# Performance work log

Hardware: AMD Instinct MI355X
Metric: run time of the kernel (lower is better)

## Reference

```python
import jax, jax.numpy as jnp
import numpy as np

N_NODES = 100000


def sage_conv(x, src, dst, W_l, b_l, W_r, n_nodes):
    # mean-aggregate source neighbors onto destination nodes (PyG SAGEConv, aggr='mean')
    agg = jax.ops.segment_sum(x[src], dst, num_segments=n_nodes)          # [N, d_in]
    cnt = jax.ops.segment_sum(jnp.ones((src.shape[0], 1), x.dtype), dst,
                              num_segments=n_nodes)                        # [N, 1]
    agg = agg / jnp.maximum(cnt, 1.0)  # isolated nodes -> 0, as in scatter-mean
    # out = lin_l(agg) + lin_r(x); bias lives in lin_l
    return agg @ W_l + b_l + x @ W_r


def setup_inputs() -> dict:
    key = jax.random.key(0)
    ks = jax.random.split(key, 12)
    d_in, h1, h2, h3 = 256, 256, 128, 1
    x = jax.random.normal(ks[0], (N_NODES, d_in), dtype=jnp.float32)
    edge_index = jax.random.randint(ks[1], (2, 1600000), 0, N_NODES, dtype=jnp.int64)

    def lin(k, din, dout):
        s = 1.0 / np.sqrt(din)
        return jax.random.uniform(k, (din, dout), jnp.float32, -s, s)

    return {
        "x": x,
        "edge_index": edge_index,
        "Wl1": lin(ks[2], d_in, h1), "bl1": jnp.zeros((h1,), jnp.float32), "Wr1": lin(ks[3], d_in, h1),
        "Wl2": lin(ks[4], h1, h2),  "bl2": jnp.zeros((h2,), jnp.float32), "Wr2": lin(ks[5], h1, h2),
        "Wl3": lin(ks[6], h2, h3),  "bl3": jnp.zeros((h3,), jnp.float32), "Wr3": lin(ks[7], h2, h3),
    }


def reference(x, edge_index, Wl1, bl1, Wr1, Wl2, bl2, Wr2, Wl3, bl3, Wr3):
    src, dst = edge_index[0], edge_index[1]
    n = x.shape[0]
    h = jax.nn.relu(sage_conv(x, src, dst, Wl1, bl1, Wr1, n))
    h = jax.nn.relu(sage_conv(h, src, dst, Wl2, bl2, Wr2, n))
    out = sage_conv(h, src, dst, Wl3, bl3, Wr3, n)
    return out  # [N, 1]
```

## Files before the change

### kernel.cpp

```cpp
#include <hip/hip_runtime.h>
#include <hip/hip_bf16.h>


typedef __attribute__((ext_vector_type(8))) short short8;
typedef __attribute__((ext_vector_type(4))) float f32x4;

__device__ __forceinline__ unsigned short f2b(float f) {
    __hip_bfloat16 h = __float2bfloat16(f);
    return *reinterpret_cast<unsigned short*>(&h);
}
__device__ __forceinline__ float b2f(unsigned short u) {
    union { unsigned int i; float f; } v; v.i = ((unsigned int)u) << 16; return v.f;
}

__global__ __launch_bounds__(256) void prep_fused(
    const float* __restrict__ x, unsigned short* __restrict__ xb,
    const float* __restrict__ Wl1, const float* __restrict__ Wr1,
    const float* __restrict__ Wl2, const float* __restrict__ Wr2,
    unsigned short* __restrict__ Wl1s, unsigned short* __restrict__ Wr1s,
    unsigned short* __restrict__ Wl2s, unsigned short* __restrict__ Wr2s,
    const int* __restrict__ dst, int* __restrict__ deg,
    unsigned short* __restrict__ rank, int E)
{
    const int b = blockIdx.x;
    const int tid = threadIdx.x;
    if (b < 25000) {
        const int i = b * 256 + tid;
        float4 v = *(const float4*)(x + (size_t)i * 4);
        ushort4 o;
        o.x = f2b(v.x); o.y = f2b(v.y); o.z = f2b(v.z); o.w = f2b(v.w);
        *(ushort4*)(xb + (size_t)i * 4) = o;
        if (tid < 64) {
            const int e = b * 64 + tid;
            if (e < E) rank[e] = (unsigned short)atomicAdd(&deg[dst[e]], 1);
        }
    } else {
        const float* W; unsigned short* O; int base, hs;
        if (b < 25256)      { W = Wl1; O = Wl1s; base = b - 25000; hs = 8; }
        else if (b < 25512) { W = Wr1; O = Wr1s; base = b - 25256; hs = 8; }
        else if (b < 25640) { W = Wl2; O = Wl2s; base = b - 25512; hs = 7; }
        else                { W = Wr2; O = Wr2s; base = b - 25640; hs = 7; }
        const int i = base * 256 + tid;
        const int k = i >> hs;
        const int h = i & ((1 << hs) - 1);
        O[((size_t)(((k >> 3) << hs) + h) << 3) + (k & 7)] = f2b(W[i]);
    }
}

__global__ __launch_bounds__(256) void scan_phaseA(int* __restrict__ a,
                                                   int* __restrict__ blockSums, int n) {
    __shared__ int sh[256];
    const int tid = threadIdx.x;
    const int base = blockIdx.x * 1024 + tid * 4;
    int v[4];
    #pragma unroll
    for (int i = 0; i < 4; ++i) v[i] = (base + i < n) ? a[base + i] : 0;
    int tsum = v[0] + v[1] + v[2] + v[3];
    sh[tid] = tsum;
    __syncthreads();
    for (int off = 1; off < 256; off <<= 1) {
        int t = (tid >= off) ? sh[tid - off] : 0;
        __syncthreads();
        sh[tid] += t;
        __syncthreads();
    }
    int run = sh[tid] - tsum;
    #pragma unroll
    for (int i = 0; i < 4; ++i) {
        if (base + i < n) a[base + i] = run;
        run += v[i];
    }
    if (tid == 255) blockSums[blockIdx.x] = sh[255];
}

__global__ __launch_bounds__(256) void scan_phaseB(int* __restrict__ bs, int nb) {
    __shared__ int sh[256];
    const int tid = threadIdx.x;
    int v = (tid < nb) ? bs[tid] : 0;
    sh[tid] = v;
    __syncthreads();
    for (int off = 1; off < 256; off <<= 1) {
        int t = (tid >= off) ? sh[tid - off] : 0;
        __syncthreads();
        sh[tid] += t;
        __syncthreads();
    }
    if (tid < nb) bs[tid] = sh[tid] - v;
}

__global__ __launch_bounds__(256) void scan_phaseC(int* __restrict__ a,
                                                   const int* __restrict__ bs, int n) {
    const int base = blockIdx.x * 1024 + threadIdx.x * 4;
    const int add = bs[blockIdx.x];
    #pragma unroll
    for (int i = 0; i < 4; ++i)
        if (base + i < n) a[base + i] += add;
}

__global__ __launch_bounds__(256) void gemm_l1_fill(
    const unsigned short* __restrict__ Xb,
    const unsigned short* __restrict__ Wsw_l,
    const unsigned short* __restrict__ Wsw_r,
    const float* __restrict__ bias,
    unsigned short* __restrict__ Tout,
    unsigned short* __restrict__ Abase,
    int M,
    const int* __restrict__ src, const int* __restrict__ dst,
    const int* __restrict__ starts, const unsigned short* __restrict__ rank,
    int* __restrict__ csr, int E)
{
    const int grp = blockIdx.x / 3;
    const int rem = blockIdx.x - grp * 3;
    const int tid = threadIdx.x;

    if (rem != 0) {
        const int e = (grp * 2 + rem - 1) * 256 + tid;
        if (e < E) csr[starts[dst[e]] + (int)rank[e]] = src[e];
        return;
    }

    const int H = 256;
    const int wid = tid >> 6;
    const int lane = tid & 63;
    const int quad = lane >> 4;
    const int l15 = lane & 15;
    const int col0 = (grp & 3) << 6;
    const int m0 = (grp >> 2) * 128 + wid * 32;

    const unsigned short* aptr[2];
    #pragma unroll
    for (int mt = 0; mt < 2; ++mt) {
        int r = m0 + mt * 16 + l15;
        if (r > M - 1) r = M - 1;
        aptr[mt] = Xb + ((size_t)r << 8) + (quad << 3);
    }
    const unsigned short* bptr[8];
    #pragma unroll
    for (int nt = 0; nt < 4; ++nt) {
        const int col = col0 + nt * 16 + l15;
        bptr[nt]     = Wsw_l + (((size_t)quad * H + col) << 3);
        bptr[nt + 4] = Wsw_r + (((size_t)quad * H + col) << 3);
    }

    const f32x4 zero = {0.f, 0.f, 0.f, 0.f};
    f32x4 acc[2][8];
    #pragma unroll
    for (int mt = 0; mt < 2; ++mt)
        #pragma unroll
        for (int nt = 0; nt < 8; ++nt) acc[mt][nt] = zero;

    #pragma unroll 2
    for (int ks = 0; ks < 8; ++ks) {
        short8 af[2], bf[8];
        #pragma unroll
        for (int mt = 0; mt < 2; ++mt)
            af[mt] = *(const short8*)(aptr[mt] + ks * 32);
        #pragma unroll
        for (int nt = 0; nt < 8; ++nt)
            bf[nt] = *(const short8*)(bptr[nt] + (size_t)ks * 32 * H);
        #pragma unroll
        for (int mt = 0; mt < 2; ++mt)
            #pragma unroll
            for (int nt = 0; nt < 8; ++nt)
                acc[mt][nt] = __builtin_amdgcn_mfma_f32_16x16x32_bf16(
                    af[mt], bf[nt], acc[mt][nt], 0, 0, 0);
    }

    #pragma unroll
    for (int nt = 0; nt < 4; ++nt) {
        const int colg = col0 + nt * 16 + l15;
        const float bb = bias[colg];
        #pragma unroll
        for (int mt = 0; mt < 2; ++mt) {
            const int gmb = m0 + mt * 16 + quad * 4;
            #pragma unroll
            for (int r = 0; r < 4; ++r) {
                if (gmb + r < M) {
                    Tout [(size_t)(gmb + r) * H + colg] = f2b(acc[mt][nt][r]);
                    Abase[(size_t)(gmb + r) * H + colg] = f2b(acc[mt][nt + 4][r] + bb);
                }
            }
        }
    }
}

__global__ __launch_bounds__(256) void agg256_b(
    const int* __restrict__ endoff, const int* __restrict__ csr,
    const unsigned short* __restrict__ T,
    const unsigned short* __restrict__ Abase, unsigned short* __restrict__ Xout,
    int N, int E)
{
    const int node = (int)((blockIdx.x * 256 + threadIdx.x) >> 5);
    const int lane = threadIdx.x & 31;
    if (node >= N) return;
    const int beg = endoff[node];
    const int end = (node + 1 < N) ? endoff[node + 1] : E;
    float s[8] = {0.f, 0.f, 0.f, 0.f, 0.f, 0.f, 0.f, 0.f};
    int p = beg;
    for (; p + 8 <= end; p += 8) {
        int idx[8];
        #pragma unroll
        for (int u = 0; u < 8; ++u) idx[u] = csr[p + u];
        short8 v[8];
        #pragma unroll
        for (int u = 0; u < 8; ++u)
            v[u] = *(const short8*)(T + ((size_t)idx[u] << 8) + (lane << 3));
        #pragma unroll
        for (int j = 0; j < 8; ++j) {
            float t0 = b2f((unsigned short)v[0][j]) + b2f((unsigned short)v[1][j]);
            float t1 = b2f((unsigned short)v[2][j]) + b2f((unsigned short)v[3][j]);
            float t2 = b2f((unsigned short)v[4][j]) + b2f((unsigned short)v[5][j]);
            float t3 = b2f((unsigned short)v[6][j]) + b2f((unsigned short)v[7][j]);
            s[j] += (t0 + t1) + (t2 + t3);
        }
    }
    if (p + 4 <= end) {
        const int a = csr[p], b = csr[p + 1], c = csr[p + 2], d = csr[p + 3];
        const short8 v0 = *(const short8*)(T + ((size_t)a << 8) + (lane << 3));
        const short8 v1 = *(const short8*)(T + ((size_t)b << 8) + (lane << 3));
        const short8 v2 = *(const short8*)(T + ((size_t)c << 8) + (lane << 3));
        const short8 v3 = *(const short8*)(T + ((size_t)d << 8) + (lane << 3));
        #pragma unroll
        for (int j = 0; j < 8; ++j)
            s[j] += (b2f((unsigned short)v0[j]) + b2f((unsigned short)v1[j]))
                  + (b2f((unsigned short)v2[j]) + b2f((unsigned short)v3[j]));
        p += 4;
    }
    for (; p < end; ++p) {
        const short8 v = *(const short8*)(T + ((size_t)csr[p] << 8) + (lane << 3));
        #pragma unroll
        for (int j = 0; j < 8; ++j) s[j] += b2f((unsigned short)v[j]);
    }
    const float w = 1.0f / fmaxf((float)(end - beg), 1.0f);
    const short8 bu = *(const short8*)(Abase + ((size_t)node << 8) + (lane << 3));
    short8 o;
    #pragma unroll
    for (int j = 0; j < 8; ++j)
        o[j] = (short)f2b(fmaxf(b2f((unsigned short)bu[j]) + s[j] * w, 0.f));
    *(short8*)(Xout + ((size_t)node << 8) + (lane << 3)) = o;
}

__global__ __launch_bounds__(256) void gemm_bf16(
    const unsigned short* __restrict__ Xb,
    const unsigned short* __restrict__ Wsw_l,
    const unsigned short* __restrict__ Wsw_r,
    const float* __restrict__ bias,
    unsigned short* __restrict__ Tout,
    unsigned short* __restrict__ Abase,
    int M, int H)
{
    const int tid = threadIdx.x;
    const int wid = tid >> 6;
    const int lane = tid & 63;
    const int quad = lane >> 4;
    const int l15 = lane & 15;

    const int col0 = blockIdx.x << 6;
    const int m0 = blockIdx.y * 128 + wid * 32;

    const unsigned short* aptr[2];
    #pragma unroll
    for (int mt = 0; mt < 2; ++mt) {
        int r = m0 + mt * 16 + l15;
        if (r > M - 1) r = M - 1;
        aptr[mt] = Xb + ((size_t)r << 8) + (quad << 3);
    }
    const unsigned short* bptr[8];
    #pragma unroll
    for (int nt = 0; nt < 4; ++nt) {
        const int col = col0 + nt * 16 + l15;
        bptr[nt]     = Wsw_l + (((size_t)quad * H + col) << 3);
        bptr[nt + 4] = Wsw_r + (((size_t)quad * H + col) << 3);
    }

    const f32x4 zero = {0.f, 0.f, 0.f, 0.f};
    f32x4 acc[2][8];
    #pragma unroll
    for (int mt = 0; mt < 2; ++mt)
        #pragma unroll
        for (int nt = 0; nt < 8; ++nt) acc[mt][nt] = zero;

    #pragma unroll 2
    for (int ks = 0; ks < 8; ++ks) {
        short8 af[2], bf[8];
        #pragma unroll
        for (int mt = 0; mt < 2; ++mt)
            af[mt] = *(const short8*)(aptr[mt] + ks * 32);
        #pragma unroll
        for (int nt = 0; nt < 8; ++nt)
            bf[nt] = *(const short8*)(bptr[nt] + (size_t)ks * 32 * H);
        #pragma unroll
        for (int mt = 0; mt < 2; ++mt)
            #pragma unroll
            for (int nt = 0; nt < 8; ++nt)
                acc[mt][nt] = __builtin_amdgcn_mfma_f32_16x16x32_bf16(
                    af[mt], bf[nt], acc[mt][nt], 0, 0, 0);
    }

    #pragma unroll
    for (int nt = 0; nt < 4; ++nt) {
        const int colg = col0 + nt * 16 + l15;
        const float bb = bias[colg];
        #pragma unroll
        for (int mt = 0; mt < 2; ++mt) {
            const int gmb = m0 + mt * 16 + quad * 4;
            #pragma unroll
            for (int r = 0; r < 4; ++r) {
                if (gmb + r < M) {
                    Tout [(size_t)(gmb + r) * H + colg] = f2b(acc[mt][nt][r]);
                    Abase[(size_t)(gmb + r) * H + colg] = f2b(acc[mt][nt + 4][r] + bb);
                }
            }
        }
    }
}

__global__ __launch_bounds__(256) void agg_gemv3(
    const int* __restrict__ endoff, const int* __restrict__ csr,
    const unsigned short* __restrict__ T, const unsigned short* __restrict__ Ab,
    const float* __restrict__ Wl, const float* __restrict__ Wr,
    const float* __restrict__ b,
    float* __restrict__ t3, float* __restrict__ out, int N, int E)
{
    const int node = (int)((blockIdx.x * 256 + threadIdx.x) >> 5);
    const int lane = threadIdx.x & 31;
    if (node >= N) return;
    const int beg = endoff[node];
    const int end = (node + 1 < N) ? endoff[node + 1] : E;
    float s0 = 0.f, s1 = 0.f, s2 = 0.f, s3 = 0.f;
    int p = beg;
    for (; p + 8 <= end; p += 8) {
        int idx[8];
        #pragma unroll
        for (int u = 0; u < 8; ++u) idx[u] = csr[p + u];
        ushort4 v[8];
        #pragma unroll
        for (int u = 0; u < 8; ++u)
            v[u] = *(const ushort4*)(T + ((size_t)idx[u] << 7) + (lane << 2));
        #pragma unroll
        for (int u = 0; u < 8; ++u) {
            s0 += b2f(v[u].x); s1 += b2f(v[u].y);
            s2 += b2f(v[u].z); s3 += b2f(v[u].w);
        }
    }
    if (p + 4 <= end) {
        const int a = csr[p], bb = csr[p + 1], c = csr[p + 2], d = csr[p + 3];
        ushort4 v0 = *(const ushort4*)(T + ((size_t)a << 7) + (lane << 2));
        ushort4 v1 = *(const ushort4*)(T + ((size_t)bb << 7) + (lane << 2));
        ushort4 v2 = *(const ushort4*)(T + ((size_t)c << 7) + (lane << 2));
        ushort4 v3 = *(const ushort4*)(T + ((size_t)d << 7) + (lane << 2));
        s0 += (b2f(v0.x) + b2f(v1.x)) + (b2f(v2.x) + b2f(v3.x));
        s1 += (b2f(v0.y) + b2f(v1.y)) + (b2f(v2.y) + b2f(v3.y));
        s2 += (b2f(v0.z) + b2f(v1.z)) + (b2f(v2.z) + b2f(v3.z));
        s3 += (b2f(v0.w) + b2f(v1.w)) + (b2f(v2.w) + b2f(v3.w));
        p += 4;
    }
    for (; p < end; ++p) {
        ushort4 v = *(const ushort4*)(T + ((size_t)csr[p] << 7) + (lane << 2));
        s0 += b2f(v.x); s1 += b2f(v.y); s2 += b2f(v.z); s3 += b2f(v.w);
    }
    const float w = 1.0f / fmaxf((float)(end - beg), 1.0f);
    const ushort4 bu = *(const ushort4*)(Ab + ((size_t)node << 7) + (lane << 2));
    const float h0 = fmaxf(b2f(bu.x) + s0 * w, 0.f);
    const float h1 = fmaxf(b2f(bu.y) + s1 * w, 0.f);
    const float h2 = fmaxf(b2f(bu.z) + s2 * w, 0.f);
    const float h3 = fmaxf(b2f(bu.w) + s3 * w, 0.f);

    const float4 wl = *(const float4*)(Wl + (lane << 2));
    const float4 wr = *(const float4*)(Wr + (lane << 2));
    float dl = h0 * wl.x + h1 * wl.y + h2 * wl.z + h3 * wl.w;
    float dr = h0 * wr.x + h1 * wr.y + h2 * wr.z + h3 * wr.w;
    #pragma unroll
    for (int off = 16; off > 0; off >>= 1) {
        dl += __shfl_down(dl, off, 64);
        dr += __shfl_down(dr, off, 64);
    }
    if (lane == 0) {
        t3[node] = dl;
        out[node] = dr + b[0];
    }
}

__global__ __launch_bounds__(256) void agg1(
    const int* __restrict__ endoff, const int* __restrict__ csr,
    const float* __restrict__ t3, float* __restrict__ out, int N, int E)
{
    const int i = blockIdx.x * blockDim.x + threadIdx.x;
    if (i >= N) return;
    const int beg = endoff[i];
    const int end = (i + 1 < N) ? endoff[i + 1] : E;
    int p = beg;
    float s = 0.f;
    for (; p + 4 <= end; p += 4)
        s += (t3[csr[p]] + t3[csr[p + 1]]) + (t3[csr[p + 2]] + t3[csr[p + 3]]);
    for (; p < end; ++p) s += t3[csr[p]];
    out[i] += s / fmaxf((float)(end - beg), 1.0f);
}

extern "C" void kernel_launch(void* const* d_in, const int* in_sizes, int n_in,
                              void* d_out, int out_size, void* d_ws, size_t ws_size,
                              hipStream_t stream) {
    const float* x   = (const float*)d_in[0];
    const int*   ei  = (const int*)d_in[1];
    const float* Wl1 = (const float*)d_in[2];
    const float* bl1 = (const float*)d_in[3];
    const float* Wr1 = (const float*)d_in[4];
    const float* Wl2 = (const float*)d_in[5];
    const float* bl2 = (const float*)d_in[6];
    const float* Wr2 = (const float*)d_in[7];
    const float* Wl3 = (const float*)d_in[8];
    const float* bl3 = (const float*)d_in[9];
    const float* Wr3 = (const float*)d_in[10];
    float* out = (float*)d_out;

    const int N = in_sizes[0] / 256;
    const int E = in_sizes[1] / 2;
    const int* src = ei;
    const int* dst = ei + E;

    char* W = (char*)d_ws;
    const size_t MB512 = (size_t)100000 * 512;
    unsigned short* X1b = (unsigned short*)(W);
    unsigned short* T1b = (unsigned short*)(W + MB512);
    unsigned short* A1b = (unsigned short*)(W + 2 * MB512);
    unsigned short* X2b = (unsigned short*)(W);
    unsigned short* T2b = (unsigned short*)(W + MB512);
    unsigned short* A2b = (unsigned short*)(W + MB512 + MB512 / 2);
    char* S = W + 3 * MB512;
    int*   endoff = (int*)(S);
    int*   bsums  = (int*)(S + (size_t)N * 4);
    float* t3     = (float*)(S + (size_t)N * 4 + 1024);
    int*   csr    = (int*)(S + (size_t)N * 8 + 1024);
    unsigned short* Wl1s = (unsigned short*)(S + (size_t)N * 8 + 1024 + (size_t)E * 4);
    unsigned short* Wr1s = Wl1s + 65536;
    unsigned short* Wl2s = Wr1s + 65536;
    unsigned short* Wr2s = Wl2s + 32768;
    unsigned short* rank = Wr2s + 32768;

    hipMemsetAsync(endoff, 0, (size_t)N * sizeof(int), stream);
    prep_fused<<<25768, 256, 0, stream>>>(
        x, X1b, Wl1, Wr1, Wl2, Wr2, Wl1s, Wr1s, Wl2s, Wr2s,
        dst, endoff, rank, E);
    const int nScanBlocks = (N + 1023) / 1024;
    scan_phaseA<<<nScanBlocks, 256, 0, stream>>>(endoff, bsums, N);
    scan_phaseB<<<1, 256, 0, stream>>>(bsums, nScanBlocks);
    scan_phaseC<<<nScanBlocks, 256, 0, stream>>>(endoff, bsums, N);

    gemm_l1_fill<<<3128 * 3, 256, 0, stream>>>(X1b, Wl1s, Wr1s, bl1, T1b, A1b, N,
                                               src, dst, endoff, rank, csr, E);

    agg256_b<<<(N * 32 + 255) / 256, 256, 0, stream>>>(endoff, csr, T1b, A1b, X2b, N, E);
    gemm_bf16<<<dim3(2, (N + 127) / 128), 256, 0, stream>>>(X2b, Wl2s, Wr2s, bl2,
                                                            T2b, A2b, N, 128);

    agg_gemv3<<<(N * 32 + 255) / 256, 256, 0, stream>>>(endoff, csr, T2b, A2b,
                                                        Wl3, Wr3, bl3, t3, out, N, E);
    agg1<<<(N + 255) / 256, 256, 0, stream>>>(endoff, csr, t3, out, N, E);
}
```

Before: 570.1 us.

## Stage layer-1 GEMM tiles in LDS via direct global-to-LDS loads, remap blocks

```diff
diff --git a/kernel.cpp b/kernel.cpp
--- a/kernel.cpp
+++ b/kernel.cpp
@@ -11,6 +11,13 @@
 }
 __device__ __forceinline__ float b2f(unsigned short u) {
     union { unsigned int i; float f; } v; v.i = ((unsigned int)u) << 16; return v.f;
+}
+
+__device__ __forceinline__ void gload_lds16(const unsigned short* g, unsigned short* l) {
+    __builtin_amdgcn_global_load_lds(
+        (const __attribute__((address_space(1))) unsigned int*)(const void*)g,
+        (__attribute__((address_space(3))) unsigned int*)(void*)l,
+        16, 0, 0);
 }
 
 __global__ __launch_bounds__(256) void prep_fused(
@@ -109,8 +116,9 @@
     const int* __restrict__ starts, const unsigned short* __restrict__ rank,
     int* __restrict__ csr, int E)
 {
-    const int grp = blockIdx.x / 3;
-    const int rem = blockIdx.x - grp * 3;
+    const int bid = (blockIdx.x & 7) * 1173 + (blockIdx.x >> 3);
+    const int grp = bid / 3;
+    const int rem = bid - grp * 3;
     const int tid = threadIdx.x;
 
     if (rem != 0) {
@@ -119,27 +127,34 @@
         return;
     }
 
-    const int H = 256;
+    __shared__ unsigned short smem[16384];
+
     const int wid = tid >> 6;
     const int lane = tid & 63;
     const int quad = lane >> 4;
     const int l15 = lane & 15;
     const int col0 = (grp & 3) << 6;
-    const int m0 = (grp >> 2) * 128 + wid * 32;
-
-    const unsigned short* aptr[2];
-    #pragma unroll
-    for (int mt = 0; mt < 2; ++mt) {
-        int r = m0 + mt * 16 + l15;
-        if (r > M - 1) r = M - 1;
-        aptr[mt] = Xb + ((size_t)r << 8) + (quad << 3);
-    }
-    const unsigned short* bptr[8];
-    #pragma unroll
-    for (int nt = 0; nt < 4; ++nt) {
-        const int col = col0 + nt * 16 + l15;
-        bptr[nt]     = Wsw_l + (((size_t)quad * H + col) << 3);
-        bptr[nt + 4] = Wsw_r + (((size_t)quad * H + col) << 3);
+    const int m0 = (grp >> 2) * 128;
+
+    const unsigned short* aSrc[4];
+    unsigned int aOfs[4];
+    #pragma unroll
+    for (int i = 0; i < 4; ++i) {
+        const int slot = i * 256 + tid;
+        const int r = slot >> 3, cs = slot & 7;
+        const int cg = cs ^ (r & 7);
+        aSrc[i] = Xb + ((size_t)(m0 + r) << 8) + (cg << 3);
+        aOfs[i] = (unsigned)((i * 256 + wid * 64) * 8);
+    }
+    const unsigned short* bSrc[4];
+    unsigned int bOfs[4];
+    #pragma unroll
+    for (int i = 0; i < 4; ++i) {
+        const int slot = i * 256 + tid;
+        const int mat = slot >> 9, ko = (slot >> 6) & 7, col = slot & 63;
+        const unsigned short* Wm = mat ? Wsw_r : Wsw_l;
+        bSrc[i] = Wm + (((size_t)ko * 256 + col0 + col) << 3);
+        bOfs[i] = (unsigned)(8192 + (i * 256 + wid * 64) * 8);
     }
 
     const f32x4 zero = {0.f, 0.f, 0.f, 0.f};
@@ -149,21 +164,39 @@
         #pragma unroll
         for (int nt = 0; nt < 8; ++nt) acc[mt][nt] = zero;
 
-    #pragma unroll 2
-    for (int ks = 0; ks < 8; ++ks) {
-        short8 af[2], bf[8];
-        #pragma unroll
-        for (int mt = 0; mt < 2; ++mt)
-            af[mt] = *(const short8*)(aptr[mt] + ks * 32);
-        #pragma unroll
-        for (int nt = 0; nt < 8; ++nt)
-            bf[nt] = *(const short8*)(bptr[nt] + (size_t)ks * 32 * H);
-        #pragma unroll
-        for (int mt = 0; mt < 2; ++mt)
-            #pragma unroll
-            for (int nt = 0; nt < 8; ++nt)
-                acc[mt][nt] = __builtin_amdgcn_mfma_f32_16x16x32_bf16(
-                    af[mt], bf[nt], acc[mt][nt], 0, 0, 0);
+    for (int ks = 0; ks < 4; ++ks) {
+        #pragma unroll
+        for (int i = 0; i < 4; ++i)
+            gload_lds16(aSrc[i] + ks * 64, smem + aOfs[i]);
+        #pragma unroll
+        for (int i = 0; i < 4; ++i)
+            gload_lds16(bSrc[i] + ks * 16384, smem + bOfs[i]);
+        __syncthreads();
+
+        #pragma unroll
+        for (int k32 = 0; k32 < 2; ++k32) {
+            short8 af[2], bf[8];
+            #pragma unroll
+            for (int mt = 0; mt < 2; ++mt) {
+                const int row = wid * 32 + mt * 16 + l15;
+                const int c = (k32 * 4 + quad) ^ (row & 7);
+                af[mt] = *(const short8*)(smem + ((row << 3) + c) * 8);
+            }
+            #pragma unroll
+            for (int nt = 0; nt < 4; ++nt) {
+                const int colL = nt * 16 + l15;
+                const int ko = k32 * 4 + quad;
+                bf[nt]     = *(const short8*)(smem + 8192 + ((ko << 6) + colL) * 8);
+                bf[nt + 4] = *(const short8*)(smem + 8192 + (512 + (ko << 6) + colL) * 8);
+            }
+            #pragma unroll
+            for (int mt = 0; mt < 2; ++mt)
+                #pragma unroll
+                for (int nt = 0; nt < 8; ++nt)
+                    acc[mt][nt] = __builtin_amdgcn_mfma_f32_16x16x32_bf16(
+                        af[mt], bf[nt], acc[mt][nt], 0, 0, 0);
+        }
+        __syncthreads();
     }
 
     #pragma unroll
@@ -172,12 +205,12 @@
         const float bb = bias[colg];
         #pragma unroll
         for (int mt = 0; mt < 2; ++mt) {
-            const int gmb = m0 + mt * 16 + quad * 4;
+            const int gmb = m0 + wid * 32 + mt * 16 + quad * 4;
             #pragma unroll
             for (int r = 0; r < 4; ++r) {
                 if (gmb + r < M) {
-                    Tout [(size_t)(gmb + r) * H + colg] = f2b(acc[mt][nt][r]);
-                    Abase[(size_t)(gmb + r) * H + colg] = f2b(acc[mt][nt + 4][r] + bb);
+                    Tout [(size_t)(gmb + r) * 256 + colg] = f2b(acc[mt][nt][r]);
+                    Abase[(size_t)(gmb + r) * 256 + colg] = f2b(acc[mt][nt + 4][r] + bb);
                 }
             }
         }
```

Measured after the change: 545.7 us. 4.3% less time.
